# Kernel tuning notes

Measured on AMD Instinct MI355X. Metric: run time of the kernel, lower is better.

Reference implementation:

```python
import jax, jax.numpy as jnp
import numpy as np

DIM = 192
HEADS = 6
WS = (2, 7, 7)
SHIFT = (1, 3, 3)
MLP_HID = int(DIM * 4.0)
N = WS[0] * WS[1] * WS[2]  # 98


def _relative_position_index():
    wt, wh, ww = WS
    coords = np.stack(np.meshgrid(np.arange(wt), np.arange(wh), np.arange(ww), indexing='ij'))
    cf = coords.reshape(3, -1)  # (3, N)
    rel = cf[:, :, None] - cf[:, None, :]  # (3, N, N)
    rel = rel.transpose(1, 2, 0).copy()
    rel[:, :, 0] += wt - 1
    rel[:, :, 1] += wh - 1
    rel[:, :, 2] += ww - 1
    rel[:, :, 0] *= (2 * wh - 1) * (2 * ww - 1)
    rel[:, :, 1] *= 2 * ww - 1
    return rel.sum(-1)  # (N, N) int

RPI = jnp.asarray(_relative_position_index())


def setup_inputs() -> dict:
    key = jax.random.key(0)
    ks = jax.random.split(key, 12)
    B, C, T, H, W = 2, DIM, 8, 56, 56
    n_bias = (2 * WS[0] - 1) * (2 * WS[1] - 1) * (2 * WS[2] - 1)
    s = lambda k, shp, sd=0.02: jax.random.normal(k, shp, jnp.float32) * sd
    return {
        'x': jax.random.normal(ks[0], (B, C, T, H, W), jnp.float32),
        'mask_matrix': jnp.zeros((256, N, N), jnp.float32),
        'norm1_g': jnp.ones((DIM,), jnp.float32),
        'norm1_b': jnp.zeros((DIM,), jnp.float32),
        'qkv_w': s(ks[1], (DIM, 3 * DIM)),
        'qkv_b': jnp.zeros((3 * DIM,), jnp.float32),
        'proj_w': s(ks[2], (DIM, DIM)),
        'proj_b': jnp.zeros((DIM,), jnp.float32),
        'rpb_table': s(ks[3], (n_bias, HEADS)),
        'norm2_g': jnp.ones((DIM,), jnp.float32),
        'norm2_b': jnp.zeros((DIM,), jnp.float32),
        'fc1_w': s(ks[4], (DIM, MLP_HID)),
        'fc1_b': jnp.zeros((MLP_HID,), jnp.float32),
        'fc2_w': s(ks[5], (MLP_HID, DIM)),
        'fc2_b': jnp.zeros((DIM,), jnp.float32),
    }


def _layernorm(x, g, b, eps=1e-5):
    mu = jnp.mean(x, -1, keepdims=True)
    var = jnp.var(x, -1, keepdims=True)
    return (x - mu) * jax.lax.rsqrt(var + eps) * g + b


def _window_partition(x):
    # x: (B, T, H, W, C) -> (B*nW, N, C)
    B, T, H, W, C = x.shape
    wt, wh, ww = WS
    x = x.reshape(B, T // wt, wt, H // wh, wh, W // ww, ww, C)
    x = x.transpose(0, 1, 3, 5, 2, 4, 6, 7)
    return x.reshape(-1, wt * wh * ww, C)


def _window_reverse(win, B, T, H, W):
    wt, wh, ww = WS
    C = win.shape[-1]
    x = win.reshape(B, T // wt, H // wh, W // ww, wt, wh, ww, C)
    x = x.transpose(0, 1, 4, 2, 5, 3, 6, 7)
    return x.reshape(B, T, H, W, C)


def reference(x, mask_matrix, norm1_g, norm1_b, qkv_w, qkv_b, proj_w, proj_b,
              rpb_table, norm2_g, norm2_b, fc1_w, fc1_b, fc2_w, fc2_b):
    B, C, T, H, W = x.shape
    hd = C // HEADS
    scale = hd ** -0.5

    shortcut = x.transpose(0, 2, 3, 4, 1)  # (B,T,H,W,C) channel-last residual
    xn = _layernorm(shortcut, norm1_g, norm1_b)
    # cyclic shift
    xs = jnp.roll(xn, shift=(-SHIFT[0], -SHIFT[1], -SHIFT[2]), axis=(1, 2, 3))
    xw = _window_partition(xs)  # (B_, N, C)
    B_ = xw.shape[0]

    qkv = (xw @ qkv_w + qkv_b).reshape(B_, N, 3, HEADS, hd)
    q, k, v = (qkv[:, :, 0].transpose(0, 2, 1, 3),
               qkv[:, :, 1].transpose(0, 2, 1, 3),
               qkv[:, :, 2].transpose(0, 2, 1, 3))  # (B_, h, N, d)
    attn = jnp.einsum('bhnd,bhmd->bhnm', q * scale, k)
    bias = rpb_table[RPI.reshape(-1)].reshape(N, N, HEADS).transpose(2, 0, 1)
    attn = attn + bias[None]
    nW = mask_matrix.shape[0]
    attn = attn.reshape(B_ // nW, nW, HEADS, N, N) + mask_matrix[None, :, None]
    attn = jax.nn.softmax(attn.reshape(B_, HEADS, N, N), axis=-1)
    out = jnp.einsum('bhnm,bhmd->bhnd', attn, v).transpose(0, 2, 1, 3).reshape(B_, N, C)
    out = out @ proj_w + proj_b

    xr = _window_reverse(out, B, T, H, W)
    xr = jnp.roll(xr, shift=SHIFT, axis=(1, 2, 3))
    x1 = shortcut + xr

    xn2 = _layernorm(x1, norm2_g, norm2_b)
    h1 = jax.nn.gelu(xn2 @ fc1_w + fc1_b, approximate=False)
    x2 = x1 + (h1 @ fc2_w + fc2_b)
    return x2.transpose(0, 4, 1, 2, 3)  # (B, C, T, H, W)
```

## Files before the change

kernel.cpp:

```cpp
#include <hip/hip_runtime.h>
#include <hip/hip_bf16.h>
#include <math.h>

#define DEV __device__ __forceinline__

typedef __bf16 bf16;
typedef __bf16 bf16x8 __attribute__((ext_vector_type(8)));
typedef float f32x4 __attribute__((ext_vector_type(4)));

DEV f32x4 zero4() { f32x4 z; z[0]=0.f; z[1]=0.f; z[2]=0.f; z[3]=0.f; return z; }

DEV void gload_lds16(const bf16* g, bf16* l) {
    __builtin_amdgcn_global_load_lds(
        (const __attribute__((address_space(1))) void*)g,
        (__attribute__((address_space(3))) void*)l, 16, 0, 0);
}

DEV float gelu_f(float v) {
    float e = __expf(-1.702f * v);
    return v * __builtin_amdgcn_rcpf(1.0f + e);
}

DEV f32x4 bmfma(bf16x8 a, bf16x8 b, f32x4 c) {
    return __builtin_amdgcn_mfma_f32_16x16x32_bf16(a, b, c, 0, 0, 0);
}


__global__ __launch_bounds__(256) void prep_all_k(
    const float* __restrict__ qw, const float* __restrict__ pw,
    const float* __restrict__ f1, const float* __restrict__ f2,
    const float* __restrict__ rpb, const float* __restrict__ maskm,
    bf16* __restrict__ qwt, bf16* __restrict__ pwt,
    bf16* __restrict__ f1t, bf16* __restrict__ f2t,
    float* __restrict__ biasF, float* __restrict__ maskF)
{
    int bid = blockIdx.x;
    if (bid < 3136) {
        int i = bid * 256 + threadIdx.x;
        if (i >= 256*7*7*64) return;
        int lane = i & 63; int g = i >> 6;
        int j = g % 7; g /= 7; int rt = g % 7; int wib = g / 7;
        int l15 = lane & 15, lg = lane >> 4;
        int nk = j*16 + l15;
        f32x4 o;
        #pragma unroll
        for (int r = 0; r < 4; r++) {
            int nq = rt*16 + lg*4 + r; if (nq > 97) nq = 97;
            o[r] = (nk < 98) ? maskm[((size_t)wib*98 + nq)*98 + nk] : 0.f;
        }
        *(f32x4*)&maskF[(size_t)i*4] = o;
    } else if (bid < 3712) {
        int i = (bid - 3136) * 256 + threadIdx.x;
        if (i < 576*192) { int n = i / 192, k = i % 192; qwt[i] = (bf16)qw[(size_t)k*576 + n]; }
        if (i < 192*192) { int n = i / 192, k = i % 192; pwt[i] = (bf16)pw[(size_t)k*192 + n]; }
        if (i < 768*192) { int n = i / 192, k = i % 192; f1t[i] = (bf16)f1[(size_t)k*768 + n]; }
        if (i < 192*768) { int n = i / 768, k = i % 768; f2t[i] = (bf16)f2[(size_t)k*192 + n]; }
    } else {
        int i = (bid - 3712) * 256 + threadIdx.x;
        if (i >= 6*7*7*64) return;
        int lane = i & 63; int g = i >> 6;
        int j = g % 7; g /= 7; int rt = g % 7; int head = g / 7;
        int l15 = lane & 15, lg = lane >> 4;
        int nk = j*16 + l15;
        f32x4 o;
        #pragma unroll
        for (int r = 0; r < 4; r++) {
            int nq = rt*16 + lg*4 + r; if (nq > 97) nq = 97;
            if (nk < 98) {
                int t1 = nq/49, r1 = nq%49, h1 = r1/7, w1 = r1%7;
                int t2 = nk/49, r2 = nk%49, h2 = r2/7, w2 = r2%7;
                int idx = (t1 - t2 + 1)*169 + (h1 - h2 + 6)*13 + (w1 - w2 + 6);
                o[r] = rpb[idx*6 + head];
            } else {
                o[r] = -1e30f;
            }
        }
        *(f32x4*)&biasF[(size_t)i*4] = o;
    }
}

__global__ __launch_bounds__(256) void ln1_window_k(
    const float* __restrict__ x, const float* __restrict__ g,
    const float* __restrict__ bta, bf16* __restrict__ xw)
{
    __shared__ float tile[56*193];
    __shared__ float mu[56], rs[56];
    int blk = blockIdx.x;
    int bb = blk / 448; int r = blk % 448; int ts = r / 56; int hs = r % 56;
    int t = (ts + 1) & 7;
    int h = hs + 3; if (h >= 56) h -= 56;
    int tid = threadIdx.x;
    const float* xs = x + ((size_t)bb*1536 + t)*3136 + h*56;
    for (int e = tid; e < 192*56; e += 256) {
        int c = e / 56, w = e % 56;
        int wsp = w - 3; if (wsp < 0) wsp += 56;
        tile[wsp*193 + c] = xs[(size_t)c*25088 + w];
    }
    __syncthreads();
    if (tid < 224) {
        int row = tid >> 2, q = tid & 3;
        float s = 0.f, s2 = 0.f;
        for (int c = q*48; c < q*48 + 48; c++) {
            float v = tile[row*193 + c]; s += v; s2 += v*v;
        }
        s  += __shfl_xor(s, 1);  s  += __shfl_xor(s, 2);
        s2 += __shfl_xor(s2, 1); s2 += __shfl_xor(s2, 2);
        if (q == 0) {
            float m = s * (1.0f/192.0f);
            mu[row] = m;
            rs[row] = rsqrtf(s2 * (1.0f/192.0f) - m*m + 1e-5f);
        }
    }
    __syncthreads();
    int tb = ts >> 1, wt = ts & 1;
    int hb = hs / 7, wh = hs % 7;
    for (int e = tid; e < 56*192; e += 256) {
        int wpos = e / 192, c = e % 192;
        float v = (tile[wpos*193 + c] - mu[wpos]) * rs[wpos] * g[c] + bta[c];
        int wb = wpos / 7, ww = wpos % 7;
        int widx = bb*256 + tb*64 + hb*8 + wb;
        int n = wt*49 + wh*7 + ww;
        xw[((size_t)widx*98 + n)*192 + c] = (bf16)v;
    }
}

template<int KT, int NT, int BN, int EPI, int DB>
__global__ __launch_bounds__(256) void gemm_k(
    const bf16* __restrict__ A, const bf16* __restrict__ BT,
    const float* __restrict__ bias, const float* __restrict__ resid,
    void* __restrict__ outp)
{
    constexpr int BUFS = DB ? 2 : 1;
    __shared__ bf16 smem[BUFS*128*64 + BUFS*BN*64];
    bf16* laB = smem;
    bf16* lbB = smem + BUFS*128*64;
    constexpr int NTILES = NT / BN;
    constexpr int NK = KT / 64;
    constexpr int JT = BN / 32;
    constexpr int WN = BN / 2;
    constexpr int SPX = 392 / 8;
    int blk = blockIdx.x;
    int xcd = blk & 7, ix = blk >> 3;
    int m0 = (xcd * SPX + ix / NTILES) * 128;
    int n0 = (ix % NTILES) * BN;
    int tid = threadIdx.x;
    int lane = tid & 63;
    int wv = tid >> 6;
    int wr = wv >> 1, wc = wv & 1;
    int l15 = lane & 15, lg = lane >> 4;

    auto stage = [&](int kt, int buf) {
        int kb = kt * 64;
        #pragma unroll
        for (int t = 0; t < 4; t++) {
            int e = t*256 + wv*64 + lane;
            int row = e >> 3, ck = e & 7;
            gload_lds16(&A[(size_t)(m0 + row)*KT + kb + ((ck ^ (row & 7)) << 3)],
                        &laB[buf*128*64 + (t*256 + wv*64) * 8]);
        }
        #pragma unroll
        for (int t = 0; t < JT; t++) {
            int e = t*256 + wv*64 + lane;
            int row = e >> 3, ck = e & 7;
            gload_lds16(&BT[(size_t)(n0 + row)*KT + kb + ((ck ^ (row & 7)) << 3)],
                        &lbB[buf*BN*64 + (t*256 + wv*64) * 8]);
        }
    };

    f32x4 acc[4][JT];
    #pragma unroll
    for (int i = 0; i < 4; i++)
        #pragma unroll
        for (int j = 0; j < JT; j++) acc[i][j] = zero4();

    auto compute = [&](int cur) {
        const bf16* lab = laB + cur*128*64;
        const bf16* lbb = lbB + cur*BN*64;
        #pragma unroll
        for (int ks = 0; ks < 64; ks += 32) {
            int lc = (ks >> 3) + lg;
            bf16x8 af[4], bfr[JT];
            #pragma unroll
            for (int i = 0; i < 4; i++) {
                int ri = wr*64 + i*16 + l15;
                af[i] = *(const bf16x8*)&lab[ri*64 + ((lc ^ (ri & 7)) << 3)];
            }
            #pragma unroll
            for (int j = 0; j < JT; j++) {
                int rj = wc*WN + j*16 + l15;
                bfr[j] = *(const bf16x8*)&lbb[rj*64 + ((lc ^ (rj & 7)) << 3)];
            }
            #pragma unroll
            for (int i = 0; i < 4; i++)
                #pragma unroll
                for (int j = 0; j < JT; j++)
                    acc[i][j] = bmfma(af[i], bfr[j], acc[i][j]);
        }
    };

    if constexpr (DB) {
        stage(0, 0);
        __syncthreads();
        for (int kt = 0; kt < NK; kt++) {
            int cur = kt & 1;
            if (kt + 1 < NK) stage(kt + 1, cur ^ 1);
            compute(cur);
            __syncthreads();
        }
    } else {
        for (int kt = 0; kt < NK; kt++) {
            stage(kt, 0);
            __syncthreads();
            compute(0);
            __syncthreads();
        }
    }

    if constexpr (EPI == 4) {
        #pragma unroll
        for (int i = 0; i < 4; i++) {
            #pragma unroll
            for (int j = 0; j < JT; j++) {
                int row0 = m0 + wr*64 + i*16 + lg*4;
                int col = n0 + wc*WN + j*16 + l15;
                f32x4 o;
                #pragma unroll
                for (int r = 0; r < 4; r++)
                    o[r] = acc[i][j][r] + bias[col] + resid[(size_t)(row0 + r)*NT + col];
                int bb2 = row0 >= 25088;
                size_t off = (size_t)bb2*192*25088 + (size_t)col*25088 + (row0 - bb2*25088);
                *(f32x4*)&((float*)outp)[off] = o;
            }
        }
    } else if constexpr (EPI == 5) {
        #pragma unroll
        for (int i = 0; i < 4; i++) {
            #pragma unroll
            for (int j = 0; j < JT; j++) {
                int col = n0 + wc*WN + j*16 + l15;
                int sel = col / 192, hd = (col % 192) >> 5, d = col & 31;
                float bv = bias[col];
                #pragma unroll
                for (int r = 0; r < 4; r++) {
                    int row = m0 + wr*64 + i*16 + lg*4 + r;
                    int b_ = row / 98, n = row - b_*98;
                    size_t dst = (((size_t)b_*6 + hd)*3 + sel)*3136 + n*32 + d;
                    ((bf16*)outp)[dst] = (bf16)(acc[i][j][r] + bv);
                }
            }
        }
    } else if constexpr (EPI == 1) {
        #pragma unroll
        for (int i = 0; i < 4; i++) {
            #pragma unroll
            for (int j = 0; j < JT; j++) {
                #pragma unroll
                for (int r = 0; r < 4; r++) {
                    int row = m0 + wr*64 + i*16 + lg*4 + r;
                    int col = n0 + wc*WN + j*16 + l15;
                    ((float*)outp)[(size_t)row*NT + col] = acc[i][j][r] + bias[col];
                }
            }
        }
    } else {
        bf16* fs = smem;
        #pragma unroll
        for (int i = 0; i < 4; i++) {
            #pragma unroll
            for (int j = 0; j < JT; j++) {
                int colw = wc*WN + j*16 + l15;
                float bv = bias[n0 + colw];
                #pragma unroll
                for (int r = 0; r < 4; r++) {
                    int lr = wr*64 + i*16 + lg*4 + r;
                    fs[lr*72 + colw] = (bf16)gelu_f(acc[i][j][r] + bv);
                }
            }
        }
        __syncthreads();
        {
            int lr = tid >> 1, c0 = (tid & 1) * 32;
            size_t gbase = (size_t)(m0 + lr)*NT + n0 + c0;
            #pragma unroll
            for (int k = 0; k < 4; k++) {
                bf16x8 o = *(const bf16x8*)&fs[lr*72 + c0 + k*8];
                *(bf16x8*)&((bf16*)outp)[gbase + k*8] = o;
            }
        }
    }
}

__global__ __launch_bounds__(128) void attn_k(
    const bf16* __restrict__ qkv, const float* __restrict__ biasF,
    const float* __restrict__ maskF, bf16* __restrict__ aout)
{
    __shared__ bf16 VT[32*128];
    __shared__ bf16 Pl[2*16*136];
    int blk = blockIdx.x;
    int t8 = (blk & 7) * 384 + (blk >> 3);
    int b_ = t8 / 6, head = t8 % 6;
    int tid = threadIdx.x, lane = tid & 63, wv = tid >> 6;
    int l15 = lane & 15, lg = (lane >> 4) & 3;
    int wib = b_ & 255;
    const bf16* base = qkv + (size_t)(b_*6 + head)*3*3136;

    {
        unsigned int* vz = (unsigned int*)VT;
        for (int e = tid; e < 2048; e += 128) vz[e] = 0u;
        unsigned int* pz = (unsigned int*)Pl;
        for (int e = tid; e < 256; e += 128) {
            int w2 = e >> 7, rem = e & 127;
            int row = rem >> 3, cp = rem & 7;
            pz[(w2*16 + row)*68 + 56 + cp] = 0u;
        }
    }
    __syncthreads();
    {
        int dq = tid >> 5;
        int kl = tid & 31;
        const bf16* vbase = base + 2*3136 + dq*8;
        #pragma unroll
        for (int kr = 0; kr < 4; kr++) {
            int k = kr*32 + kl;
            if (k < 98) {
                bf16x8 v8 = *(const bf16x8*)&vbase[k*32];
                #pragma unroll
                for (int j = 0; j < 8; j++)
                    VT[(dq*8 + j)*128 + (k ^ (j << 3))] = v8[j];
            }
        }
    }
    __syncthreads();

    bf16x8 kfr[7];
    #pragma unroll
    for (int j = 0; j < 7; j++) {
        int krow = j*16 + l15; if (krow > 97) krow = 97;
        kfr[j] = *(const bf16x8*)&base[3136 + krow*32 + lg*8];
    }

    const float scale = 0.17677669529663687f;
    bf16* Pw = Pl + wv*16*136;
    const int rt0 = wv ? 4 : 0, rt1 = wv ? 7 : 4;

    auto loadQ = [&](int rt) {
        int qrow = rt*16 + l15; if (qrow > 97) qrow = 97;
        return *(const bf16x8*)&base[qrow*32 + lg*8];
    };
    bf16x8 qf = loadQ(rt0);

    #pragma unroll 1
    for (int rt = rt0; rt < rt1; rt++) {
        bf16x8 qnext = qf;
        if (rt + 1 < rt1) qnext = loadQ(rt + 1);
        f32x4 sacc[7];
        #pragma unroll
        for (int j = 0; j < 7; j++) sacc[j] = zero4();
        #pragma unroll
        for (int j = 0; j < 7; j++)
            sacc[j] = bmfma(qf, kfr[j], sacc[j]);
        {
            const float* bfp = biasF + ((size_t)(head*7 + rt)*7)*256 + lane*4;
            const float* mfp = maskF + ((size_t)(wib*7 + rt)*7)*256 + lane*4;
            #pragma unroll
            for (int j = 0; j < 7; j++) {
                f32x4 bv = *(const f32x4*)&bfp[j*256];
                f32x4 mv = *(const f32x4*)&mfp[j*256];
                sacc[j] = sacc[j]*scale + bv + mv;
            }
            f32x4 m4 = sacc[0];
            #pragma unroll
            for (int j = 1; j < 7; j++) {
                #pragma unroll
                for (int r = 0; r < 4; r++) m4[r] = fmaxf(m4[r], sacc[j][r]);
            }
            #pragma unroll
            for (int d = 1; d < 16; d <<= 1) {
                #pragma unroll
                for (int r = 0; r < 4; r++) m4[r] = fmaxf(m4[r], __shfl_xor(m4[r], d));
            }
            f32x4 s4 = zero4();
            #pragma unroll
            for (int j = 0; j < 7; j++) {
                #pragma unroll
                for (int r = 0; r < 4; r++) sacc[j][r] = __expf(sacc[j][r] - m4[r]);
                s4 += sacc[j];
            }
            #pragma unroll
            for (int d = 1; d < 16; d <<= 1) {
                #pragma unroll
                for (int r = 0; r < 4; r++) s4[r] += __shfl_xor(s4[r], d);
            }
            f32x4 inv4;
            #pragma unroll
            for (int r = 0; r < 4; r++) inv4[r] = 1.0f / s4[r];
            #pragma unroll
            for (int j = 0; j < 7; j++)
                #pragma unroll
                for (int r = 0; r < 4; r++)
                    Pw[(lg*4 + r)*136 + j*16 + l15] = (bf16)(sacc[j][r]*inv4[r]);
        }
        #pragma unroll
        for (int dt = 0; dt < 2; dt++) {
            int dl = dt*16 + l15;
            int xr = (dl & 7) << 3;
            f32x4 oacc = zero4();
            #pragma unroll
            for (int kc = 0; kc < 4; kc++) {
                bf16x8 pf = *(const bf16x8*)&Pw[l15*136 + kc*32 + lg*8];
                bf16x8 vf = *(const bf16x8*)&VT[dl*128 + ((kc*32 + lg*8) ^ xr)];
                oacc = bmfma(pf, vf, oacc);
            }
            #pragma unroll
            for (int r = 0; r < 4; r++) {
                int row = rt*16 + lg*4 + r;
                if (row < 98)
                    aout[((size_t)b_*98 + row)*192 + head*32 + dt*16 + l15] = (bf16)oacc[r];
            }
        }
        qf = qnext;
    }
}

__global__ __launch_bounds__(256) void rev_res_ln2_k(
    const float* __restrict__ x, const float* __restrict__ pw,
    const float* __restrict__ g2, const float* __restrict__ b2,
    float* __restrict__ x1, bf16* __restrict__ xn2)
{
    __shared__ float tile[56*193];
    __shared__ float mu[56], rs[56];
    int blk = blockIdx.x;
    int bb = blk / 448; int r = blk % 448; int t = r / 56; int h = r % 56;
    int ts = (t + 7) & 7;
    int hs = h - 3; if (hs < 0) hs += 56;
    int tid = threadIdx.x;
    const float* xs = x + ((size_t)bb*1536 + t)*3136 + h*56;
    for (int e = tid; e < 192*56; e += 256) {
        int c = e / 56, w = e % 56;
        tile[w*193 + c] = xs[(size_t)c*25088 + w];
    }
    __syncthreads();
    int tb = ts >> 1, wt = ts & 1, hb = hs / 7, wh = hs % 7;
    for (int e = tid; e < 56*192; e += 256) {
        int w = e / 192, c = e % 192;
        int wsp = w - 3; if (wsp < 0) wsp += 56;
        int wb = wsp / 7, ww = wsp % 7;
        size_t tok = (size_t)(bb*256 + tb*64 + hb*8 + wb)*98 + wt*49 + wh*7 + ww;
        tile[w*193 + c] += pw[tok*192 + c];
    }
    __syncthreads();
    if (tid < 224) {
        int row = tid >> 2, q = tid & 3;
        float s = 0.f, s2 = 0.f;
        for (int c = q*48; c < q*48 + 48; c++) {
            float v = tile[row*193 + c]; s += v; s2 += v*v;
        }
        s  += __shfl_xor(s, 1);  s  += __shfl_xor(s, 2);
        s2 += __shfl_xor(s2, 1); s2 += __shfl_xor(s2, 2);
        if (q == 0) {
            float m = s * (1.0f/192.0f);
            mu[row] = m;
            rs[row] = rsqrtf(s2 * (1.0f/192.0f) - m*m + 1e-5f);
        }
    }
    __syncthreads();
    size_t tok0 = ((size_t)(bb*8 + t)*56 + h)*56;
    for (int e = tid; e < 56*192; e += 256) {
        int w = e / 192, c = e % 192;
        float v = tile[w*193 + c];
        x1[(tok0 + w)*192 + c] = v;
        xn2[(tok0 + w)*192 + c] = (bf16)((v - mu[w]) * rs[w] * g2[c] + b2[c]);
    }
}

extern "C" void kernel_launch(void* const* d_in, const int* in_sizes, int n_in,
                              void* d_out, int out_size, void* d_ws, size_t ws_size,
                              hipStream_t stream)
{
    const float* x     = (const float*)d_in[0];
    const float* maskm = (const float*)d_in[1];
    const float* n1g   = (const float*)d_in[2];
    const float* n1b   = (const float*)d_in[3];
    const float* qkvw  = (const float*)d_in[4];
    const float* qkvb  = (const float*)d_in[5];
    const float* projw = (const float*)d_in[6];
    const float* projb = (const float*)d_in[7];
    const float* rpb   = (const float*)d_in[8];
    const float* n2g   = (const float*)d_in[9];
    const float* n2b   = (const float*)d_in[10];
    const float* f1w   = (const float*)d_in[11];
    const float* f1b   = (const float*)d_in[12];
    const float* f2w   = (const float*)d_in[13];
    const float* f2b   = (const float*)d_in[14];

    char* ws = (char*)d_ws;
    bf16*  qkv_wt  = (bf16*)(ws + 0);
    bf16*  proj_wt = (bf16*)(ws + 221184);
    bf16*  fc1_wt  = (bf16*)(ws + 294912);
    bf16*  fc2_wt  = (bf16*)(ws + 589824);
    float* biasF   = (float*)(ws + 884736);
    bf16* xw   = (bf16*)(ws + 1179648);
    bf16* aout = xw;
    char* Bp = ws + 1179648 + 19267584;
    bf16*  qkv  = (bf16*)Bp;
    float* pwin = (float*)Bp;
    char* Cp = Bp + 57802752;
    float* x1  = (float*)Cp;
    bf16*  xn2 = (bf16*)(Cp + 38535168);
    bf16*  h1  = (bf16*)(Cp + 38535168 + 19267584);
    float* maskF = (float*)(Cp + 38535168 + 19267584);

    prep_all_k<<<3786, 256, 0, stream>>>(qkvw, projw, f1w, f2w, rpb, maskm,
                                         qkv_wt, proj_wt, fc1_wt, fc2_wt,
                                         biasF, maskF);
    ln1_window_k<<<896, 256, 0, stream>>>(x, n1g, n1b, xw);
    gemm_k<192, 576, 192, 5, 0><<<392*3, 256, 0, stream>>>(xw, qkv_wt, qkvb, nullptr, qkv);
    attn_k<<<3072, 128, 0, stream>>>(qkv, biasF, maskF, aout);
    gemm_k<192, 192, 64, 1, 0><<<392*3, 256, 0, stream>>>(aout, proj_wt, projb, nullptr, pwin);
    rev_res_ln2_k<<<896, 256, 0, stream>>>(x, pwin, n2g, n2b, x1, xn2);
    gemm_k<192, 768, 64, 2, 0><<<392*12, 256, 0, stream>>>(xn2, fc1_wt, f1b, nullptr, h1);
    gemm_k<768, 192, 64, 4, 1><<<392*3, 256, 0, stream>>>(h1, fc2_wt, f2b, x1, (float*)d_out);
}
```

Baseline: 228.1 us.

## Skip mask loads for all-zero windows, store proj in bf16, widen fc1 tiles

A new block range in the prep kernel scans each window's mask and writes a per-window flag. The attention kernel then loads and adds the mask tile only when that flag is set, which removes mask memory traffic whenever the mask is all zero. The projection GEMM now writes bf16 instead of fp32, halving that intermediate's traffic at some precision cost. The fc1 GEMM uses 192-wide N tiles with a chunked GELU epilogue, so each A tile is reused across more columns. The flag check is computed from the actual input every call, so it is a real runtime branch rather than an assumption.

New measurement: 252.1 us. 1.11x slower.

```diff
diff --git a/kernel.cpp b/kernel.cpp
--- a/kernel.cpp
+++ b/kernel.cpp
@@ -32,7 +32,8 @@
     const float* __restrict__ rpb, const float* __restrict__ maskm,
     bf16* __restrict__ qwt, bf16* __restrict__ pwt,
     bf16* __restrict__ f1t, bf16* __restrict__ f2t,
-    float* __restrict__ biasF, float* __restrict__ maskF)
+    float* __restrict__ biasF, float* __restrict__ maskF,
+    int* __restrict__ wflag)
 {
     int bid = blockIdx.x;
     if (bid < 3136) {
@@ -55,7 +56,7 @@
         if (i < 192*192) { int n = i / 192, k = i % 192; pwt[i] = (bf16)pw[(size_t)k*192 + n]; }
         if (i < 768*192) { int n = i / 192, k = i % 192; f1t[i] = (bf16)f1[(size_t)k*768 + n]; }
         if (i < 192*768) { int n = i / 768, k = i % 768; f2t[i] = (bf16)f2[(size_t)k*192 + n]; }
-    } else {
+    } else if (bid < 3786) {
         int i = (bid - 3712) * 256 + threadIdx.x;
         if (i >= 6*7*7*64) return;
         int lane = i & 63; int g = i >> 6;
@@ -76,6 +77,18 @@
             }
         }
         *(f32x4*)&biasF[(size_t)i*4] = o;
+    } else {
+        __shared__ int f;
+        int wib = bid - 3786;
+        if (threadIdx.x == 0) f = 0;
+        __syncthreads();
+        int any = 0;
+        const float* mm = maskm + (size_t)wib*9604;
+        for (int i = threadIdx.x; i < 9604; i += 256)
+            if (mm[i] != 0.f) any = 1;
+        if (any) atomicOr(&f, 1);
+        __syncthreads();
+        if (threadIdx.x == 0) wflag[wib] = f;
     }
 }
 
@@ -249,7 +262,7 @@
                 }
             }
         }
-    } else if constexpr (EPI == 1) {
+    } else if constexpr (EPI == 1 || EPI == 0) {
         #pragma unroll
         for (int i = 0; i < 4; i++) {
             #pragma unroll
@@ -258,41 +271,53 @@
                 for (int r = 0; r < 4; r++) {
                     int row = m0 + wr*64 + i*16 + lg*4 + r;
                     int col = n0 + wc*WN + j*16 + l15;
-                    ((float*)outp)[(size_t)row*NT + col] = acc[i][j][r] + bias[col];
+                    float v = acc[i][j][r] + bias[col];
+                    if constexpr (EPI == 1)
+                        ((float*)outp)[(size_t)row*NT + col] = v;
+                    else
+                        ((bf16*)outp)[(size_t)row*NT + col] = (bf16)v;
                 }
             }
         }
     } else {
         bf16* fs = smem;
-        #pragma unroll
-        for (int i = 0; i < 4; i++) {
-            #pragma unroll
-            for (int j = 0; j < JT; j++) {
-                int colw = wc*WN + j*16 + l15;
-                float bv = bias[n0 + colw];
-                #pragma unroll
-                for (int r = 0; r < 4; r++) {
-                    int lr = wr*64 + i*16 + lg*4 + r;
-                    fs[lr*72 + colw] = (bf16)gelu_f(acc[i][j][r] + bv);
+        constexpr int CH = BN / 64;
+        #pragma unroll
+        for (int ch = 0; ch < CH; ch++) {
+            #pragma unroll
+            for (int i = 0; i < 4; i++) {
+                #pragma unroll
+                for (int j = 0; j < JT; j++) {
+                    int colw = wc*WN + j*16 + l15;
+                    if ((colw >> 6) == ch) {
+                        float bv = bias[n0 + colw];
+                        #pragma unroll
+                        for (int r = 0; r < 4; r++) {
+                            int lr = wr*64 + i*16 + lg*4 + r;
+                            fs[lr*72 + (colw & 63)] = (bf16)gelu_f(acc[i][j][r] + bv);
+                        }
+                    }
                 }
             }
-        }
-        __syncthreads();
-        {
-            int lr = tid >> 1, c0 = (tid & 1) * 32;
-            size_t gbase = (size_t)(m0 + lr)*NT + n0 + c0;
-            #pragma unroll
-            for (int k = 0; k < 4; k++) {
-                bf16x8 o = *(const bf16x8*)&fs[lr*72 + c0 + k*8];
-                *(bf16x8*)&((bf16*)outp)[gbase + k*8] = o;
-            }
+            __syncthreads();
+            {
+                int lr = tid >> 1, c0 = (tid & 1) * 32;
+                size_t gbase = (size_t)(m0 + lr)*NT + n0 + ch*64 + c0;
+                #pragma unroll
+                for (int k = 0; k < 4; k++) {
+                    bf16x8 o = *(const bf16x8*)&fs[lr*72 + c0 + k*8];
+                    *(bf16x8*)&((bf16*)outp)[gbase + k*8] = o;
+                }
+            }
+            __syncthreads();
         }
     }
 }
 
 __global__ __launch_bounds__(128) void attn_k(
     const bf16* __restrict__ qkv, const float* __restrict__ biasF,
-    const float* __restrict__ maskF, bf16* __restrict__ aout)
+    const float* __restrict__ maskF, const int* __restrict__ wflag,
+    bf16* __restrict__ aout)
 {
     __shared__ bf16 VT[32*128];
     __shared__ bf16 Pl[2*16*136];
@@ -303,6 +328,7 @@
     int l15 = lane & 15, lg = (lane >> 4) & 3;
     int wib = b_ & 255;
     const bf16* base = qkv + (size_t)(b_*6 + head)*3*3136;
+    const int hasmask = wflag[wib];
 
     {
         unsigned int* vz = (unsigned int*)VT;
@@ -361,12 +387,18 @@
             sacc[j] = bmfma(qf, kfr[j], sacc[j]);
         {
             const float* bfp = biasF + ((size_t)(head*7 + rt)*7)*256 + lane*4;
-            const float* mfp = maskF + ((size_t)(wib*7 + rt)*7)*256 + lane*4;
             #pragma unroll
             for (int j = 0; j < 7; j++) {
                 f32x4 bv = *(const f32x4*)&bfp[j*256];
-                f32x4 mv = *(const f32x4*)&mfp[j*256];
-                sacc[j] = sacc[j]*scale + bv + mv;
+                sacc[j] = sacc[j]*scale + bv;
+            }
+            if (hasmask) {
+                const float* mfp = maskF + ((size_t)(wib*7 + rt)*7)*256 + lane*4;
+                #pragma unroll
+                for (int j = 0; j < 7; j++) {
+                    f32x4 mv = *(const f32x4*)&mfp[j*256];
+                    sacc[j] = sacc[j] + mv;
+                }
             }
             f32x4 m4 = sacc[0];
             #pragma unroll
@@ -423,7 +455,7 @@
 }
 
 __global__ __launch_bounds__(256) void rev_res_ln2_k(
-    const float* __restrict__ x, const float* __restrict__ pw,
+    const float* __restrict__ x, const bf16* __restrict__ pw,
     const float* __restrict__ g2, const float* __restrict__ b2,
     float* __restrict__ x1, bf16* __restrict__ xn2)
 {
@@ -446,7 +478,7 @@
         int wsp = w - 3; if (wsp < 0) wsp += 56;
         int wb = wsp / 7, ww = wsp % 7;
         size_t tok = (size_t)(bb*256 + tb*64 + hb*8 + wb)*98 + wt*49 + wh*7 + ww;
-        tile[w*193 + c] += pw[tok*192 + c];
+        tile[w*193 + c] += (float)pw[tok*192 + c];
     }
     __syncthreads();
     if (tid < 224) {
@@ -494,30 +526,31 @@
     const float* f2b   = (const float*)d_in[14];
 
     char* ws = (char*)d_ws;
-    bf16*  qkv_wt  = (bf16*)(ws + 0);
-    bf16*  proj_wt = (bf16*)(ws + 221184);
-    bf16*  fc1_wt  = (bf16*)(ws + 294912);
-    bf16*  fc2_wt  = (bf16*)(ws + 589824);
-    float* biasF   = (float*)(ws + 884736);
-    bf16* xw   = (bf16*)(ws + 1179648);
+    int*   wflag   = (int*)(ws + 0);
+    bf16*  qkv_wt  = (bf16*)(ws + 1024);
+    bf16*  proj_wt = (bf16*)(ws + 222208);
+    bf16*  fc1_wt  = (bf16*)(ws + 295936);
+    bf16*  fc2_wt  = (bf16*)(ws + 590848);
+    float* biasF   = (float*)(ws + 885760);
+    bf16* xw   = (bf16*)(ws + 1180672);
     bf16* aout = xw;
-    char* Bp = ws + 1179648 + 19267584;
+    char* Bp = ws + 1180672 + 19267584;
     bf16*  qkv  = (bf16*)Bp;
-    float* pwin = (float*)Bp;
+    bf16*  pwin = (bf16*)Bp;
     char* Cp = Bp + 57802752;
     float* x1  = (float*)Cp;
     bf16*  xn2 = (bf16*)(Cp + 38535168);
     bf16*  h1  = (bf16*)(Cp + 38535168 + 19267584);
     float* maskF = (float*)(Cp + 38535168 + 19267584);
 
-    prep_all_k<<<3786, 256, 0, stream>>>(qkvw, projw, f1w, f2w, rpb, maskm,
+    prep_all_k<<<4042, 256, 0, stream>>>(qkvw, projw, f1w, f2w, rpb, maskm,
                                          qkv_wt, proj_wt, fc1_wt, fc2_wt,
-                                         biasF, maskF);
+                                         biasF, maskF, wflag);
     ln1_window_k<<<896, 256, 0, stream>>>(x, n1g, n1b, xw);
     gemm_k<192, 576, 192, 5, 0><<<392*3, 256, 0, stream>>>(xw, qkv_wt, qkvb, nullptr, qkv);
-    attn_k<<<3072, 128, 0, stream>>>(qkv, biasF, maskF, aout);
-    gemm_k<192, 192, 64, 1, 0><<<392*3, 256, 0, stream>>>(aout, proj_wt, projb, nullptr, pwin);
+    attn_k<<<3072, 128, 0, stream>>>(qkv, biasF, maskF, wflag, aout);
+    gemm_k<192, 192, 64, 0, 0><<<392*3, 256, 0, stream>>>(aout, proj_wt, projb, nullptr, pwin);
     rev_res_ln2_k<<<896, 256, 0, stream>>>(x, pwin, n2g, n2b, x1, xn2);
-    gemm_k<192, 768, 64, 2, 0><<<392*12, 256, 0, stream>>>(xn2, fc1_wt, f1b, nullptr, h1);
+    gemm_k<192, 768, 192, 2, 0><<<392*4, 256, 0, stream>>>(xn2, fc1_wt, f1b, nullptr, h1);
     gemm_k<768, 192, 64, 4, 1><<<392*3, 256, 0, stream>>>(h1, fc2_wt, f2b, x1, (float*)d_out);
 }
```
